# Optimization experiments

Hardware: AMD Instinct MI355X
Metric: run time of the kernel (lower is better)

The kernel has to match this reference:

```python
import jax, jax.numpy as jnp
import numpy as np

N_NODES = 100000


def gcn_conv(x, W, b, src, dst, n):
    """PyG GCNConv with default add_self_loops and symmetric normalization."""
    xw = x @ W  # [N, out]
    loop = jnp.arange(n, dtype=src.dtype)
    s = jnp.concatenate([src, loop])  # source j
    d = jnp.concatenate([dst, loop])  # target i
    deg = jax.ops.segment_sum(jnp.ones_like(d, dtype=xw.dtype), d, num_segments=n)
    dinv = jnp.where(deg > 0, jax.lax.rsqrt(deg), 0.0)
    norm = dinv[s] * dinv[d]  # [E+N]
    msg = xw[s] * norm[:, None]
    out = jax.ops.segment_sum(msg, d, num_segments=n)
    return out + b


def setup_inputs() -> dict:
    key = jax.random.key(0)
    ks = jax.random.split(key, 9)
    n, e, f = N_NODES, 1600000, 512
    x = jax.random.normal(ks[0], (n, f), dtype=jnp.float32)
    edge_index = jax.random.randint(ks[1], (2, e), 0, n, dtype=jnp.int32)
    y = jax.random.uniform(ks[2], (n, 1), dtype=jnp.float32)
    W1 = jax.random.normal(ks[3], (f, 64), dtype=jnp.float32) / np.sqrt(f)
    b1 = jnp.zeros((64,), jnp.float32)
    W2 = jax.random.normal(ks[4], (64, 256), dtype=jnp.float32) / np.sqrt(64)
    b2 = jnp.zeros((256,), jnp.float32)
    W3 = jax.random.normal(ks[5], (256, 1), dtype=jnp.float32) / np.sqrt(256)
    b3 = jnp.zeros((1,), jnp.float32)
    return {"x": x, "edge_index": edge_index, "y": y,
            "W1": W1, "b1": b1, "W2": W2, "b2": b2, "W3": W3, "b3": b3}


def reference(x, edge_index, y, W1, b1, W2, b2, W3, b3):
    n = x.shape[0]
    src, dst = edge_index[0], edge_index[1]
    h = jax.nn.relu(gcn_conv(x, W1, b1, src, dst, n))
    # dropout is identity in eval mode
    h = jax.nn.relu(gcn_conv(h, W2, b2, src, dst, n))
    z = gcn_conv(h, W3, b3, src, dst, n)  # logits [N, 1]
    # BCE(sigmoid(z), y), computed stably via log-sigmoid
    loss = -(y * jax.nn.log_sigmoid(z) + (1.0 - y) * jax.nn.log_sigmoid(-z))
    return jnp.mean(loss)
```

## Files before the change

### kernel.cpp

```cpp
#include <hip/hip_runtime.h>
#include <math.h>

typedef __attribute__((ext_vector_type(8))) short s16x8;
typedef __attribute__((ext_vector_type(4))) float f32x4;

__device__ inline ushort f2bf(float f) {
    union { float f; unsigned u; } v; v.f = f;
    unsigned r = v.u + 0x7FFF + ((v.u >> 16) & 1);
    return (ushort)(r >> 16);
}
__device__ inline float bf2f(ushort h) {
    union { unsigned u; float f; } v; v.u = ((unsigned)h) << 16;
    return v.f;
}
__device__ inline float bfLo(unsigned u) {
    union { unsigned x; float f; } v; v.x = u << 16; return v.f;
}
__device__ inline float bfHi(unsigned u) {
    union { unsigned x; float f; } v; v.x = u & 0xFFFF0000u; return v.f;
}


__global__ void hist_kernel(const int* __restrict__ dst, int E, int* __restrict__ cnt) {
    int e = blockIdx.x * blockDim.x + threadIdx.x;
    if (e < E) atomicAdd(&cnt[dst[e]], 1);
}

__global__ void alloc_kernel(const int* __restrict__ cnt, int* __restrict__ row_start,
                             float* __restrict__ dinv, int* __restrict__ total, int N) {
    int i = blockIdx.x * blockDim.x + threadIdx.x;
    int lane = threadIdx.x & 63;
    int c = (i < N) ? cnt[i] : 0;
    int inc = c;
#pragma unroll
    for (int o = 1; o < 64; o <<= 1) {
        int v = __shfl_up(inc, o, 64);
        if (lane >= o) inc += v;
    }
    int wsum = __shfl(inc, 63, 64);
    int base = 0;
    if (lane == 0) base = atomicAdd(total, wsum);
    base = __shfl(base, 0, 64);
    if (i < N) {
        row_start[i] = base + inc - c;
        dinv[i] = rsqrtf((float)(c + 1));
    }
}

__global__ void scatter_kernel(const int* __restrict__ src, const int* __restrict__ dst, int E,
                               const int* __restrict__ row_start, int* __restrict__ cursor,
                               int* __restrict__ csr) {
    int e = blockIdx.x * blockDim.x + threadIdx.x;
    if (e < E) {
        int d = dst[e];
        int p = row_start[d] + atomicAdd(&cursor[d], 1);
        csr[p] = src[e];
    }
}

__global__ void wsplit_kernel(const float* __restrict__ W, ushort* __restrict__ wt_hi,
                              ushort* __restrict__ wt_lo) {
    int idx = blockIdx.x * blockDim.x + threadIdx.x;
    if (idx < 64 * 512) {
        int n = idx & 63, k = idx >> 6;
        float f = W[k * 64 + n];
        ushort h = f2bf(f);
        wt_hi[n * 512 + k] = h;
        wt_lo[n * 512 + k] = f2bf(f - bf2f(h));
    }
}

__global__ void w2split_kernel(const float* __restrict__ W, ushort* __restrict__ wt_hi,
                               ushort* __restrict__ wt_lo) {
    int idx = blockIdx.x * blockDim.x + threadIdx.x;
    if (idx < 64 * 256) {
        int n = idx & 255, k = idx >> 8;
        float f = W[k * 256 + n];
        ushort h = f2bf(f);
        wt_hi[n * 64 + k] = h;
        wt_lo[n * 64 + k] = f2bf(f - bf2f(h));
    }
}

__global__ __launch_bounds__(256, 3) void gemm1_kernel(const float* __restrict__ x,
                                                       const ushort* __restrict__ wt_hi,
                                                       const ushort* __restrict__ wt_lo,
                                                       const float* __restrict__ dinv,
                                                       ushort* __restrict__ out, int N) {
    __shared__ __align__(16) short xs_hi[128 * 64];
    __shared__ __align__(16) short xs_lo[128 * 64];
    __shared__ __align__(16) short ws_hi[64 * 64];
    __shared__ __align__(16) short ws_lo[64 * 64];

    const int tid = threadIdx.x;
    const int nodeBase = blockIdx.x * 128;
    const int wave = tid >> 6, lane = tid & 63;
    const int m16 = lane & 15, quad = lane >> 4;

    f32x4 acc[2][4];
#pragma unroll
    for (int mt = 0; mt < 2; mt++)
#pragma unroll
        for (int nt = 0; nt < 4; nt++) acc[mt][nt] = (f32x4){0.f, 0.f, 0.f, 0.f};

    for (int kc = 0; kc < 512; kc += 64) {
        __syncthreads();
#pragma unroll
        for (int i = 0; i < 4; i++) {
            int f = tid + i * 256;
            int node = f >> 3, g = f & 7;
            int gn = nodeBase + node;
            if (gn >= N) gn = N - 1;
            const float4 a = *(const float4*)(x + (size_t)gn * 512 + kc + g * 8);
            const float4 b = *(const float4*)(x + (size_t)gn * 512 + kc + g * 8 + 4);
            float ff[8] = {a.x, a.y, a.z, a.w, b.x, b.y, b.z, b.w};
            union { ushort u[8]; uint4 v; } H, L;
#pragma unroll
            for (int j = 0; j < 8; j++) {
                ushort h = f2bf(ff[j]);
                H.u[j] = h;
                L.u[j] = f2bf(ff[j] - bf2f(h));
            }
            int gp = (g + node) & 7;
            *(uint4*)&xs_hi[node * 64 + gp * 8] = H.v;
            *(uint4*)&xs_lo[node * 64 + gp * 8] = L.v;
        }
#pragma unroll
        for (int i = 0; i < 2; i++) {
            int f = tid + i * 256;
            int n = f >> 3, g = f & 7;
            int gp = (g + n) & 7;
            *(uint4*)&ws_hi[n * 64 + gp * 8] =
                *(const uint4*)(wt_hi + (size_t)n * 512 + kc + g * 8);
            *(uint4*)&ws_lo[n * 64 + gp * 8] =
                *(const uint4*)(wt_lo + (size_t)n * 512 + kc + g * 8);
        }
        __syncthreads();
#pragma unroll
        for (int ck = 0; ck < 2; ck++) {
            s16x8 Ah[2], Al[2];
#pragma unroll
            for (int mt = 0; mt < 2; mt++) {
                int row = (wave * 2 + mt) * 16 + m16;
                int gp = (ck * 4 + quad + row) & 7;
                Ah[mt] = *(s16x8*)&xs_hi[row * 64 + gp * 8];
                Al[mt] = *(s16x8*)&xs_lo[row * 64 + gp * 8];
            }
#pragma unroll
            for (int nt = 0; nt < 4; nt++) {
                int n = nt * 16 + m16;
                int gp = (ck * 4 + quad + n) & 7;
                s16x8 Bh = *(s16x8*)&ws_hi[n * 64 + gp * 8];
                s16x8 Bl = *(s16x8*)&ws_lo[n * 64 + gp * 8];
#pragma unroll
                for (int mt = 0; mt < 2; mt++) {
                    acc[mt][nt] = __builtin_amdgcn_mfma_f32_16x16x32_bf16(Ah[mt], Bh, acc[mt][nt], 0, 0, 0);
                    acc[mt][nt] = __builtin_amdgcn_mfma_f32_16x16x32_bf16(Ah[mt], Bl, acc[mt][nt], 0, 0, 0);
                    acc[mt][nt] = __builtin_amdgcn_mfma_f32_16x16x32_bf16(Al[mt], Bh, acc[mt][nt], 0, 0, 0);
                }
            }
        }
    }
#pragma unroll
    for (int mt = 0; mt < 2; mt++) {
#pragma unroll
        for (int r = 0; r < 4; r++) {
            int gn = nodeBase + (wave * 2 + mt) * 16 + quad * 4 + r;
            if (gn < N) {
                float di = dinv[gn];
#pragma unroll
                for (int nt = 0; nt < 4; nt++)
                    out[(size_t)gn * 64 + nt * 16 + m16] = f2bf(di * acc[mt][nt][r]);
            }
        }
    }
}

template <int RELU, int BIAS, int PREMUL>
__global__ void agg64bf_kernel(const ushort* __restrict__ in, ushort* __restrict__ out,
                               const int* __restrict__ row_start, const int* __restrict__ cnt,
                               const int* __restrict__ csr, const float* __restrict__ dinv,
                               const float* __restrict__ bias, int N) {
    int gw = (int)((blockIdx.x * (size_t)blockDim.x + threadIdx.x) >> 6);
    int lane = threadIdx.x & 63;
    if (gw >= N) return;
    float acc = bf2f(in[(size_t)gw * 64 + lane]);
    int s = row_start[gw];
    int c = cnt[gw];
    int e = 0;
    for (; e + 8 <= c; e += 8) {
        int j0 = csr[s + e + 0], j1 = csr[s + e + 1], j2 = csr[s + e + 2], j3 = csr[s + e + 3];
        int j4 = csr[s + e + 4], j5 = csr[s + e + 5], j6 = csr[s + e + 6], j7 = csr[s + e + 7];
        float v0 = bf2f(in[(size_t)j0 * 64 + lane]);
        float v1 = bf2f(in[(size_t)j1 * 64 + lane]);
        float v2 = bf2f(in[(size_t)j2 * 64 + lane]);
        float v3 = bf2f(in[(size_t)j3 * 64 + lane]);
        float v4 = bf2f(in[(size_t)j4 * 64 + lane]);
        float v5 = bf2f(in[(size_t)j5 * 64 + lane]);
        float v6 = bf2f(in[(size_t)j6 * 64 + lane]);
        float v7 = bf2f(in[(size_t)j7 * 64 + lane]);
        acc += ((v0 + v1) + (v2 + v3)) + ((v4 + v5) + (v6 + v7));
    }
    for (; e < c; e++) {
        int j = csr[s + e];
        acc += bf2f(in[(size_t)j * 64 + lane]);
    }
    float di = dinv[gw];
    float v = di * acc;
    if (BIAS) v += bias[lane];
    if (RELU) v = fmaxf(v, 0.f);
    if (PREMUL) v *= di;
    out[(size_t)gw * 64 + lane] = f2bf(v);
}

__global__ __launch_bounds__(256, 2) void gemm23_kernel(const ushort* __restrict__ a2,
                                                        const ushort* __restrict__ wt2_hi,
                                                        const ushort* __restrict__ wt2_lo,
                                                        const float* __restrict__ b2,
                                                        const float* __restrict__ W3,
                                                        const float* __restrict__ dinv,
                                                        float* __restrict__ r, int N) {
    const int tid = threadIdx.x;
    const int wave = tid >> 6, lane = tid & 63;
    const int m16 = lane & 15, quad = lane >> 4;
    const int rowBase = blockIdx.x * 128 + wave * 32;

    s16x8 A[2][2];
#pragma unroll
    for (int mt = 0; mt < 2; mt++) {
        int gn = rowBase + mt * 16 + m16;
        if (gn >= N) gn = N - 1;
        const ushort* ap = a2 + (size_t)gn * 64 + quad * 8;
#pragma unroll
        for (int ck = 0; ck < 2; ck++)
            A[mt][ck] = *(const s16x8*)(ap + ck * 32);
    }

    f32x4 acc[2][16];
#pragma unroll
    for (int mt = 0; mt < 2; mt++)
#pragma unroll
        for (int nt = 0; nt < 16; nt++) acc[mt][nt] = (f32x4){0.f, 0.f, 0.f, 0.f};

#pragma unroll
    for (int nt = 0; nt < 16; nt++) {
        int n = nt * 16 + m16;
        const ushort* bh = wt2_hi + (size_t)n * 64 + quad * 8;
        const ushort* bl = wt2_lo + (size_t)n * 64 + quad * 8;
        s16x8 Bh0 = *(const s16x8*)(bh);
        s16x8 Bh1 = *(const s16x8*)(bh + 32);
        s16x8 Bl0 = *(const s16x8*)(bl);
        s16x8 Bl1 = *(const s16x8*)(bl + 32);
        acc[0][nt] = __builtin_amdgcn_mfma_f32_16x16x32_bf16(A[0][0], Bh0, acc[0][nt], 0, 0, 0);
        acc[1][nt] = __builtin_amdgcn_mfma_f32_16x16x32_bf16(A[1][0], Bh0, acc[1][nt], 0, 0, 0);
        acc[0][nt] = __builtin_amdgcn_mfma_f32_16x16x32_bf16(A[0][1], Bh1, acc[0][nt], 0, 0, 0);
        acc[1][nt] = __builtin_amdgcn_mfma_f32_16x16x32_bf16(A[1][1], Bh1, acc[1][nt], 0, 0, 0);
        acc[0][nt] = __builtin_amdgcn_mfma_f32_16x16x32_bf16(A[0][0], Bl0, acc[0][nt], 0, 0, 0);
        acc[1][nt] = __builtin_amdgcn_mfma_f32_16x16x32_bf16(A[1][0], Bl0, acc[1][nt], 0, 0, 0);
        acc[0][nt] = __builtin_amdgcn_mfma_f32_16x16x32_bf16(A[0][1], Bl1, acc[0][nt], 0, 0, 0);
        acc[1][nt] = __builtin_amdgcn_mfma_f32_16x16x32_bf16(A[1][1], Bl1, acc[1][nt], 0, 0, 0);
    }

    float bv[16], wv[16];
#pragma unroll
    for (int nt = 0; nt < 16; nt++) {
        bv[nt] = b2[nt * 16 + m16];
        wv[nt] = W3[nt * 16 + m16];
    }
#pragma unroll
    for (int mt = 0; mt < 2; mt++) {
#pragma unroll
        for (int rr = 0; rr < 4; rr++) {
            float p = 0.f;
#pragma unroll
            for (int nt = 0; nt < 16; nt++) {
                float v = fmaxf(acc[mt][nt][rr] + bv[nt], 0.f);
                p = fmaf(v, wv[nt], p);
            }
#pragma unroll
            for (int off = 1; off < 16; off <<= 1) p += __shfl_xor(p, off, 64);
            int gn = rowBase + mt * 16 + quad * 4 + rr;
            if (m16 == 0 && gn < N) r[gn] = dinv[gn] * p;
        }
    }
}

__global__ void loss_kernel(const float* __restrict__ r, const float* __restrict__ dinv,
                            const int* __restrict__ row_start, const int* __restrict__ cnt,
                            const int* __restrict__ csr, const float* __restrict__ y,
                            const float* __restrict__ b3, float* __restrict__ out,
                            int N, float invN) {
    int i = blockIdx.x * blockDim.x + threadIdx.x;
    float loss = 0.f;
    if (i < N) {
        float aedge = r[i];
        int s = row_start[i], c = cnt[i];
        int e = 0;
        for (; e + 4 <= c; e += 4) {
            int j0 = csr[s + e + 0], j1 = csr[s + e + 1];
            int j2 = csr[s + e + 2], j3 = csr[s + e + 3];
            aedge += (r[j0] + r[j1]) + (r[j2] + r[j3]);
        }
        for (; e < c; e++) aedge += r[csr[s + e]];
        float z = dinv[i] * aedge + b3[0];
        float yv = y[i];
        float L = log1pf(expf(-fabsf(z)));
        float spz  = fmaxf(z, 0.f) + L;
        float spnz = fmaxf(-z, 0.f) + L;
        loss = yv * spnz + (1.f - yv) * spz;
    }
#pragma unroll
    for (int off = 32; off > 0; off >>= 1) loss += __shfl_down(loss, off, 64);
    __shared__ float red[4];
    int lane = threadIdx.x & 63, wave = threadIdx.x >> 6;
    if (lane == 0) red[wave] = loss;
    __syncthreads();
    if (threadIdx.x == 0)
        atomicAdd(out, (red[0] + red[1] + red[2] + red[3]) * invN);
}

extern "C" void kernel_launch(void* const* d_in, const int* in_sizes, int n_in,
                              void* d_out, int out_size, void* d_ws, size_t ws_size,
                              hipStream_t stream) {
    const float* x  = (const float*)d_in[0];
    const int*   ei = (const int*)d_in[1];
    const float* y  = (const float*)d_in[2];
    const float* W1 = (const float*)d_in[3];
    const float* b1 = (const float*)d_in[4];
    const float* W2 = (const float*)d_in[5];
    const float* b2 = (const float*)d_in[6];
    const float* W3 = (const float*)d_in[7];
    const float* b3 = (const float*)d_in[8];

    const int N = in_sizes[2];
    const int E = in_sizes[1] / 2;
    const int* src  = ei;
    const int* dstp = ei + E;

    char* w = (char*)d_ws;
    int*    cnt       = (int*)w;    w += (size_t)N * 4;
    int*    cursor    = (int*)w;    w += (size_t)N * 4;
    int*    total     = (int*)w;    w += 16;
    int*    row_start = (int*)w;    w += (size_t)N * 4;
    float*  dinv      = (float*)w;  w += (size_t)N * 4;
    int*    csr       = (int*)w;    w += (size_t)E * 4;
    ushort* wt_hi     = (ushort*)w; w += (size_t)64 * 512 * 2;
    ushort* wt_lo     = (ushort*)w; w += (size_t)64 * 512 * 2;
    ushort* wt2_hi    = (ushort*)w; w += (size_t)256 * 64 * 2;
    ushort* wt2_lo    = (ushort*)w; w += (size_t)256 * 64 * 2;
    ushort* pbuf      = (ushort*)w; w += (size_t)N * 64 * 2;
    ushort* qbuf      = (ushort*)w; w += (size_t)N * 64 * 2;
    float*  rbuf      = (float*)w;  w += (size_t)N * 4;

    hipMemsetAsync(cnt, 0, (size_t)N * 8 + 16, stream);
    hipMemsetAsync(d_out, 0, sizeof(float), stream);

    const int tb = 256;
    wsplit_kernel<<<(64 * 512 + tb - 1) / tb, tb, 0, stream>>>(W1, wt_hi, wt_lo);
    w2split_kernel<<<(64 * 256 + tb - 1) / tb, tb, 0, stream>>>(W2, wt2_hi, wt2_lo);
    hist_kernel<<<(E + tb - 1) / tb, tb, 0, stream>>>(dstp, E, cnt);
    alloc_kernel<<<(N + tb - 1) / tb, tb, 0, stream>>>(cnt, row_start, dinv, total, N);
    scatter_kernel<<<(E + tb - 1) / tb, tb, 0, stream>>>(src, dstp, E, row_start, cursor, csr);

    gemm1_kernel<<<(N + 127) / 128, 256, 0, stream>>>(x, wt_hi, wt_lo, dinv, pbuf, N);
    agg64bf_kernel<1, 1, 1><<<(N + 3) / 4, 256, 0, stream>>>(pbuf, qbuf, row_start, cnt, csr, dinv, b1, N);
    agg64bf_kernel<0, 0, 0><<<(N + 3) / 4, 256, 0, stream>>>(qbuf, pbuf, row_start, cnt, csr, dinv, nullptr, N);

    gemm23_kernel<<<(N + 127) / 128, 256, 0, stream>>>(pbuf, wt2_hi, wt2_lo, b2, W3, dinv, rbuf, N);

    loss_kernel<<<(N + tb - 1) / tb, tb, 0, stream>>>(rbuf, dinv, row_start, cnt, csr, y, b3,
                                                      (float*)d_out, N, 1.0f / N);
}
```

Baseline: 675.8 us.

## Split neighbor gathers across lane quads in aggregation and use wave-per-node loss

The 64-wide aggregation kernel now has each wave process four edges at once. Each 16-lane quad loads 4 bf16 features (8 bytes) of one neighbor row, and the partial sums are combined with cross-quad shuffles, so more independent row gathers are in flight per wave. The loss kernel moves from one thread per node to one wave per node, with lanes striding over the edges and a shuffle reduction. This is meant to raise memory-level parallelism in the gather-bound stages, at the cost of predicated tails, shuffle overhead, and many idle lanes in the loss kernel, since average degree is about 16.

```diff
diff --git a/kernel.cpp b/kernel.cpp
--- a/kernel.cpp
+++ b/kernel.cpp
@@ -184,33 +184,47 @@
     int gw = (int)((blockIdx.x * (size_t)blockDim.x + threadIdx.x) >> 6);
     int lane = threadIdx.x & 63;
     if (gw >= N) return;
-    float acc = bf2f(in[(size_t)gw * 64 + lane]);
-    int s = row_start[gw];
-    int c = cnt[gw];
-    int e = 0;
-    for (; e + 8 <= c; e += 8) {
-        int j0 = csr[s + e + 0], j1 = csr[s + e + 1], j2 = csr[s + e + 2], j3 = csr[s + e + 3];
-        int j4 = csr[s + e + 4], j5 = csr[s + e + 5], j6 = csr[s + e + 6], j7 = csr[s + e + 7];
-        float v0 = bf2f(in[(size_t)j0 * 64 + lane]);
-        float v1 = bf2f(in[(size_t)j1 * 64 + lane]);
-        float v2 = bf2f(in[(size_t)j2 * 64 + lane]);
-        float v3 = bf2f(in[(size_t)j3 * 64 + lane]);
-        float v4 = bf2f(in[(size_t)j4 * 64 + lane]);
-        float v5 = bf2f(in[(size_t)j5 * 64 + lane]);
-        float v6 = bf2f(in[(size_t)j6 * 64 + lane]);
-        float v7 = bf2f(in[(size_t)j7 * 64 + lane]);
-        acc += ((v0 + v1) + (v2 + v3)) + ((v4 + v5) + (v6 + v7));
-    }
-    for (; e < c; e++) {
-        int j = csr[s + e];
-        acc += bf2f(in[(size_t)j * 64 + lane]);
-    }
+    const int m16 = lane & 15;
+    const int quad = lane >> 4;
+
+    const int s = row_start[gw];
+    const int c = cnt[gw];
+    const int total = c + 1;
+
+    float a0 = 0.f, a1 = 0.f, a2v = 0.f, a3 = 0.f;
+    for (int e = 0; e < total; e += 8) {
+        int s0 = e + quad, s1 = e + 4 + quad;
+        bool v0 = s0 < total, v1 = s1 < total;
+        int j0 = gw, j1 = gw;
+        if (v0 && s0 > 0) j0 = csr[s + s0 - 1];
+        if (v1 && s1 > 0) j1 = csr[s + s1 - 1];
+        uint2 u0 = *(const uint2*)(in + (size_t)j0 * 64 + m16 * 4);
+        uint2 u1 = *(const uint2*)(in + (size_t)j1 * 64 + m16 * 4);
+        if (v0) { a0 += bfLo(u0.x); a1 += bfHi(u0.x); a2v += bfLo(u0.y); a3 += bfHi(u0.y); }
+        if (v1) { a0 += bfLo(u1.x); a1 += bfHi(u1.x); a2v += bfLo(u1.y); a3 += bfHi(u1.y); }
+    }
+    a0 += __shfl_xor(a0, 16, 64); a0 += __shfl_xor(a0, 32, 64);
+    a1 += __shfl_xor(a1, 16, 64); a1 += __shfl_xor(a1, 32, 64);
+    a2v += __shfl_xor(a2v, 16, 64); a2v += __shfl_xor(a2v, 32, 64);
+    a3 += __shfl_xor(a3, 16, 64); a3 += __shfl_xor(a3, 32, 64);
+
     float di = dinv[gw];
-    float v = di * acc;
-    if (BIAS) v += bias[lane];
-    if (RELU) v = fmaxf(v, 0.f);
-    if (PREMUL) v *= di;
-    out[(size_t)gw * 64 + lane] = f2bf(v);
+    float r0 = di * a0, r1 = di * a1, r2 = di * a2v, r3 = di * a3;
+    if (BIAS) {
+        float4 bv = *(const float4*)&bias[m16 * 4];
+        r0 += bv.x; r1 += bv.y; r2 += bv.z; r3 += bv.w;
+    }
+    if (RELU) {
+        r0 = fmaxf(r0, 0.f); r1 = fmaxf(r1, 0.f);
+        r2 = fmaxf(r2, 0.f); r3 = fmaxf(r3, 0.f);
+    }
+    if (PREMUL) { r0 *= di; r1 *= di; r2 *= di; r3 *= di; }
+    if (quad == 0) {
+        uint2 o;
+        o.x = ((unsigned)f2bf(r1) << 16) | f2bf(r0);
+        o.y = ((unsigned)f2bf(r3) << 16) | f2bf(r2);
+        *(uint2*)(out + (size_t)gw * 64 + m16 * 4) = o;
+    }
 }
 
 __global__ __launch_bounds__(256, 2) void gemm23_kernel(const ushort* __restrict__ a2,
@@ -290,29 +304,26 @@
                             const int* __restrict__ csr, const float* __restrict__ y,
                             const float* __restrict__ b3, float* __restrict__ out,
                             int N, float invN) {
-    int i = blockIdx.x * blockDim.x + threadIdx.x;
+    int gw = (int)((blockIdx.x * (size_t)blockDim.x + threadIdx.x) >> 6);
+    int lane = threadIdx.x & 63;
+    int wave = threadIdx.x >> 6;
     float loss = 0.f;
-    if (i < N) {
-        float aedge = r[i];
-        int s = row_start[i], c = cnt[i];
-        int e = 0;
-        for (; e + 4 <= c; e += 4) {
-            int j0 = csr[s + e + 0], j1 = csr[s + e + 1];
-            int j2 = csr[s + e + 2], j3 = csr[s + e + 3];
-            aedge += (r[j0] + r[j1]) + (r[j2] + r[j3]);
-        }
-        for (; e < c; e++) aedge += r[csr[s + e]];
-        float z = dinv[i] * aedge + b3[0];
-        float yv = y[i];
-        float L = log1pf(expf(-fabsf(z)));
-        float spz  = fmaxf(z, 0.f) + L;
-        float spnz = fmaxf(-z, 0.f) + L;
-        loss = yv * spnz + (1.f - yv) * spz;
-    }
-#pragma unroll
-    for (int off = 32; off > 0; off >>= 1) loss += __shfl_down(loss, off, 64);
+    if (gw < N) {
+        int s = row_start[gw], c = cnt[gw];
+        float acc = 0.f;
+        for (int e = lane; e < c; e += 64) acc += r[csr[s + e]];
+#pragma unroll
+        for (int off = 32; off > 0; off >>= 1) acc += __shfl_xor(acc, off, 64);
+        if (lane == 0) {
+            float z = dinv[gw] * (r[gw] + acc) + b3[0];
+            float yv = y[gw];
+            float L = log1pf(expf(-fabsf(z)));
+            float spz  = fmaxf(z, 0.f) + L;
+            float spnz = fmaxf(-z, 0.f) + L;
+            loss = yv * spnz + (1.f - yv) * spz;
+        }
+    }
     __shared__ float red[4];
-    int lane = threadIdx.x & 63, wave = threadIdx.x >> 6;
     if (lane == 0) red[wave] = loss;
     __syncthreads();
     if (threadIdx.x == 0)
@@ -368,6 +379,6 @@
 
     gemm23_kernel<<<(N + 127) / 128, 256, 0, stream>>>(pbuf, wt2_hi, wt2_lo, b2, W3, dinv, rbuf, N);
 
-    loss_kernel<<<(N + tb - 1) / tb, tb, 0, stream>>>(rbuf, dinv, row_start, cnt, csr, y, b3,
-                                                      (float*)d_out, N, 1.0f / N);
-}
+    loss_kernel<<<(N * 64 + tb - 1) / tb, tb, 0, stream>>>(rbuf, dinv, row_start, cnt, csr, y, b3,
+                                                           (float*)d_out, N, 1.0f / N);
+}
```

Result: slower. 966.8 us (+43.1%).
